# Kernel tuning notes

Hardware: AMD Instinct MI355X
Metric: run time of the kernel (lower is better)

Reference implementation:

```python
import jax, jax.numpy as jnp
import numpy as np

CONF_THRESH = 0.5   # foreground objectness threshold (module default)
NMS_THRESH = 0.4    # IoU suppression threshold (module default)
SCORE_THRESH = 0.3  # hard-coded max-class-score filter in forward

BS, NUM_BOXES, NUM_ATTRS = 2, 6300, 85  # 80 classes


def setup_inputs() -> dict:
    key = jax.random.key(0)
    # uniform [0,1): boxes live in the unit square and overlap heavily,
    # objectness/class scores frequently exceed the thresholds.
    x = jax.random.uniform(key, (BS, NUM_BOXES, NUM_ATTRS), dtype=jnp.float32)
    return {"x": x}


def _nms_keep(corners, scores, cls_idx, valid):
    """Per-image, per-class greedy NMS.

    corners: [N,4] (x1,y1,x2,y2), scores: [N] objectness, cls_idx: [N] int,
    valid: [N] bool. Returns keep mask [N] bool. Faithful to the torch loop:
    sort by objectness desc, greedily keep the top box of each class and
    suppress same-class boxes with IoU >= nms_thresh (torch keeps iou < t).
    """
    n = scores.shape[0]
    order = jnp.argsort(-scores)      # descending by objectness (column 4)
    rank = jnp.argsort(order)         # rank[j] = position of box j in order

    x1, y1, x2, y2 = corners[:, 0], corners[:, 1], corners[:, 2], corners[:, 3]
    area = (x2 - x1) * (y2 - y1)
    iw = jnp.maximum(jnp.minimum(x2[:, None], x2[None, :]) -
                     jnp.maximum(x1[:, None], x1[None, :]), 0.0)
    ih = jnp.maximum(jnp.minimum(y2[:, None], y2[None, :]) -
                     jnp.maximum(y1[:, None], y1[None, :]), 0.0)
    inter = iw * ih                                   # [N,N]
    iou = inter / (area[:, None] + area[None, :] - inter + 1e-16)
    same_cls = cls_idx[:, None] == cls_idx[None, :]    # [N,N]

    def body(r, keep):
        i = order[r]
        # suppress strictly lower-ranked, still-alive, same-class overlaps
        sup = (iou[i] >= NMS_THRESH) & same_cls[i] & (rank > r)
        return jnp.where(keep[i], keep & ~sup, keep)

    return jax.lax.fori_loop(0, n, body, valid)


def reference(x):
    """x: [bs, N, 5+num_classes]. Returns detections [bs, N, 8]:
    [batch_idx, x1, y1, x2, y2, p_obj, max_cls_score, cls_idx],
    zeroed for suppressed / filtered boxes (fixed-shape analogue of the
    variable-length torch output)."""
    conf_mask = x[..., 4] > CONF_THRESH
    xm = x * conf_mask[..., None].astype(x.dtype)

    # center -> corner transform
    xy, wh = xm[..., :2], xm[..., 2:4]
    corners = jnp.concatenate([xy - wh * 0.5, xy + wh * 0.5], axis=-1)  # [bs,N,4]

    p_obj = xm[..., 4]
    cls_scores = xm[..., 5:]
    max_score = jnp.max(cls_scores, axis=-1)
    cls_idx = jnp.argmax(cls_scores, axis=-1)
    valid = conf_mask & (max_score > SCORE_THRESH)

    keep = jax.vmap(_nms_keep)(corners, p_obj, cls_idx, valid)  # [bs,N] bool

    bs, n = p_obj.shape
    batch_idx = jnp.broadcast_to(
        jnp.arange(bs, dtype=x.dtype)[:, None], (bs, n))
    det = jnp.concatenate([
        batch_idx[..., None], corners, p_obj[..., None],
        max_score[..., None], cls_idx.astype(x.dtype)[..., None]], axis=-1)
    return det * keep[..., None].astype(x.dtype)
```

## Files before the change

kernel.cpp:

```cpp
#include <hip/hip_runtime.h>

#define BSZ   2
#define NBOX  6300
#define NATTR 85
#define NCLS  80
#define CAP   256

typedef unsigned long long ull;

static __device__ __forceinline__ ull mask_for(int rem) {
  if (rem <= 0) return 0ull;
  if (rem >= 64) return ~0ull;
  return (1ull << rem) - 1ull;
}

__global__ __launch_bounds__(256) void prep_kernel(
    const float* __restrict__ x,
    int* __restrict__ vcls,
    float* __restrict__ out) {
  int gid  = blockIdx.x * blockDim.x + threadIdx.x;
  int box  = gid >> 6;
  int lane = threadIdx.x & 63;

  const float* p = x + (long)box * NATTR;
  float r0 = p[lane];
  float r1 = (lane < NATTR - 64) ? p[64 + lane] : -1.0f;

  float c0 = (lane >= 5) ? r0 : -1.0f;
  float v; int vi;
  if (r1 > c0) { v = r1; vi = 64 + lane; }
  else         { v = c0; vi = lane; }

  for (int off = 32; off > 0; off >>= 1) {
    float ov = __shfl_xor(v, off);
    int   oi = __shfl_xor(vi, off);
    if (ov > v || (ov == v && oi < vi)) { v = ov; vi = oi; }
  }

  float cx  = __shfl(r0, 0), cy = __shfl(r0, 1);
  float w   = __shfl(r0, 2), h  = __shfl(r0, 3);
  float obj = __shfl(r0, 4);
  bool valid = (obj > 0.5f) && (v > 0.3f);
  int  img   = box >= NBOX ? 1 : 0;
  int  cls   = vi - 5;

  if (lane == 0) {
    vcls[box] = valid ? cls : -1;
    float4 a, b;
    if (valid) {
      float hw = w * 0.5f, hh = h * 0.5f;
      a = make_float4((float)img, cx - hw, cy - hh, cx + hw);
      b = make_float4(cy + hh, obj, v, (float)cls);
    } else {
      a = make_float4(0.f, 0.f, 0.f, 0.f);
      b = a;
    }
    float4* o = (float4*)(out + (long)box * 8);
    o[0] = a; o[1] = b;
  }
}

__global__ __launch_bounds__(256) void nms_kernel(
    const int* __restrict__ vcls,
    float* out) {
  __shared__ int   wlist[4][CAP];
  __shared__ int   wcnt[4];
  __shared__ int   sbi[CAP];
  __shared__ float ssc[CAP];
  __shared__ float px1[CAP], py1[CAP], px2[CAP], py2[CAP];
  __shared__ int   pbi[CAP];

  int bc   = blockIdx.x;
  int img  = bc / NCLS;
  int cls  = bc - img * NCLS;
  int t    = threadIdx.x;
  int lane = t & 63;
  int w    = t >> 6;
  const int* v = vcls + img * NBOX;

  int base = w * 1600;
  int vals[25];
#pragma unroll
  for (int i = 0; i < 25; i++) {
    int idx = base + i * 64 + lane;
    vals[i] = (idx < NBOX) ? v[idx] : -1;
  }
  int cnt = 0;
#pragma unroll
  for (int i = 0; i < 25; i++) {
    bool match = (vals[i] == cls);
    ull  m = __ballot(match);
    if (match) {
      int pos = cnt + __popcll(m & ((1ull << lane) - 1ull));
      if (pos < CAP) wlist[w][pos] = base + i * 64 + lane;
    }
    cnt += __popcll(m);
  }
  if (lane == 0) wcnt[w] = cnt < CAP ? cnt : CAP;
  __syncthreads();

  int off = 0, total = 0;
  for (int j = 0; j < 4; j++) {
    int c = wcnt[j];
    if (j < w) off += c;
    total += c;
  }
  int k = total < CAP ? total : CAP;
  if (k == 0) return;

  for (int j = lane; j < wcnt[w]; j += 64) {
    int d = off + j;
    if (d < CAP) sbi[d] = wlist[w][j];
  }
  __syncthreads();

  if (k <= 64) {
    if (w == 0) {
      int j = lane;
      float x1 = 0.f, y1 = 0.f, x2 = 0.f, y2 = 0.f, sc = 0.f;
      int bi = 0;
      if (j < k) {
        bi = sbi[j];
        const float4* o = (const float4*)(out + ((long)img * NBOX + bi) * 8);
        float4 a = o[0], b = o[1];
        x1 = a.y; y1 = a.z; x2 = a.w; y2 = b.x; sc = b.y;
      }
      int rank = 0;
      for (int i = 0; i < k; i++) {
        float si  = __shfl(sc, i);
        int   bii = __shfl(bi, i);
        rank += (si > sc) || (si == sc && bii < bi);
      }
      if (j >= k) rank = j;

      int r4 = rank << 2;
      x1 = __int_as_float(__builtin_amdgcn_ds_permute(r4, __float_as_int(x1)));
      y1 = __int_as_float(__builtin_amdgcn_ds_permute(r4, __float_as_int(y1)));
      x2 = __int_as_float(__builtin_amdgcn_ds_permute(r4, __float_as_int(x2)));
      y2 = __int_as_float(__builtin_amdgcn_ds_permute(r4, __float_as_int(y2)));
      bi = __builtin_amdgcn_ds_permute(r4, bi);

      float ar = (x2 - x1) * (y2 - y1);

      ull keep = mask_for(k);
      for (int r = 0; r < k - 1; r++) {
        if (!((keep >> r) & 1ull)) continue;
        float X1 = __shfl(x1, r), Y1 = __shfl(y1, r);
        float X2 = __shfl(x2, r), Y2 = __shfl(y2, r);
        float AR = __shfl(ar, r);
        float iw = fminf(X2, x2) - fmaxf(X1, x1);
        float ih = fminf(Y2, y2) - fmaxf(Y1, y1);
        iw = fmaxf(iw, 0.0f); ih = fmaxf(ih, 0.0f);
        float inter = iw * ih;
        float iou = inter / (AR + ar - inter + 1e-16f);
        keep &= ~__ballot(iou >= 0.4f && lane > r);
      }

      if (lane < k && !((keep >> lane) & 1ull)) {
        float4 z = make_float4(0.f, 0.f, 0.f, 0.f);
        float4* o = (float4*)(out + ((long)img * NBOX + bi) * 8);
        o[0] = z; o[1] = z;
      }
    }
    return;
  }

  float bx1 = 0, by1 = 0, bx2 = 0, by2 = 0, bobj = 0;
  int   bidx = 0;
  if (t < k) {
    bidx = sbi[t];
    const float4* o = (const float4*)(out + ((long)img * NBOX + bidx) * 8);
    float4 a = o[0], b = o[1];
    bx1 = a.y; by1 = a.z; bx2 = a.w; by2 = b.x; bobj = b.y;
    ssc[t] = bobj;
  }
  __syncthreads();

  if (t < k) {
    int rank = 0;
    for (int j = 0; j < k; j++) {
      float sj = ssc[j];
      rank += (sj > bobj) || (sj == bobj && sbi[j] < bidx);
    }
    px1[rank] = bx1; py1[rank] = by1;
    px2[rank] = bx2; py2[rank] = by2;
    pbi[rank] = bidx;
  }
  __syncthreads();

  if (w == 0) {
    float mx1[4], my1[4], mx2[4], my2[4], mar[4];
    int   mbi[4];
#pragma unroll
    for (int s = 0; s < 4; s++) {
      int e = s * 64 + lane;
      if (e < k) {
        mx1[s] = px1[e]; my1[s] = py1[e];
        mx2[s] = px2[e]; my2[s] = py2[e];
        mbi[s] = pbi[e];
        mar[s] = (mx2[s] - mx1[s]) * (my2[s] - my1[s]);
      } else {
        mx1[s] = 0; my1[s] = 0; mx2[s] = 0; my2[s] = 0; mar[s] = 0; mbi[s] = 0;
      }
    }
    ull km0 = mask_for(k);
    ull km1 = mask_for(k - 64);
    ull km2 = mask_for(k - 128);
    ull km3 = mask_for(k - 192);

    for (int r = 0; r < k - 1; r++) {
      ull cur = (r < 64) ? km0 : (r < 128) ? km1 : (r < 192) ? km2 : km3;
      if (!((cur >> (r & 63)) & 1ull)) continue;
      float X1 = px1[r], Y1 = py1[r], X2 = px2[r], Y2 = py2[r];
      float ar = (X2 - X1) * (Y2 - Y1);
      {
        int e = lane;
        float iw = fminf(X2, mx2[0]) - fmaxf(X1, mx1[0]);
        float ih = fminf(Y2, my2[0]) - fmaxf(Y1, my1[0]);
        iw = fmaxf(iw, 0.0f); ih = fmaxf(ih, 0.0f);
        float inter = iw * ih;
        float iou = inter / (ar + mar[0] - inter + 1e-16f);
        km0 &= ~__ballot(iou >= 0.4f && e > r && e < k);
      }
      if (k > 64) {
        int e = 64 + lane;
        float iw = fminf(X2, mx2[1]) - fmaxf(X1, mx1[1]);
        float ih = fminf(Y2, my2[1]) - fmaxf(Y1, my1[1]);
        iw = fmaxf(iw, 0.0f); ih = fmaxf(ih, 0.0f);
        float inter = iw * ih;
        float iou = inter / (ar + mar[1] - inter + 1e-16f);
        km1 &= ~__ballot(iou >= 0.4f && e > r && e < k);
      }
      if (k > 128) {
        int e = 128 + lane;
        float iw = fminf(X2, mx2[2]) - fmaxf(X1, mx1[2]);
        float ih = fminf(Y2, my2[2]) - fmaxf(Y1, my1[2]);
        iw = fmaxf(iw, 0.0f); ih = fmaxf(ih, 0.0f);
        float inter = iw * ih;
        float iou = inter / (ar + mar[2] - inter + 1e-16f);
        km2 &= ~__ballot(iou >= 0.4f && e > r && e < k);
      }
      if (k > 192) {
        int e = 192 + lane;
        float iw = fminf(X2, mx2[3]) - fmaxf(X1, mx1[3]);
        float ih = fminf(Y2, my2[3]) - fmaxf(Y1, my1[3]);
        iw = fmaxf(iw, 0.0f); ih = fmaxf(ih, 0.0f);
        float inter = iw * ih;
        float iou = inter / (ar + mar[3] - inter + 1e-16f);
        km3 &= ~__ballot(iou >= 0.4f && e > r && e < k);
      }
    }

    float4 z = make_float4(0.f, 0.f, 0.f, 0.f);
#pragma unroll
    for (int s = 0; s < 4; s++) {
      ull kms = (s == 0) ? km0 : (s == 1) ? km1 : (s == 2) ? km2 : km3;
      int e = s * 64 + lane;
      if (e < k && !((kms >> lane) & 1ull)) {
        float4* o = (float4*)(out + ((long)img * NBOX + mbi[s]) * 8);
        o[0] = z; o[1] = z;
      }
    }
  }
}

extern "C" void kernel_launch(void* const* d_in, const int* in_sizes, int n_in,
                              void* d_out, int out_size, void* d_ws, size_t ws_size,
                              hipStream_t stream) {
  const float* x = (const float*)d_in[0];
  float* out = (float*)d_out;
  int* vcls = (int*)d_ws;

  prep_kernel<<<(BSZ * NBOX * 64) / 256, 256, 0, stream>>>(x, vcls, out);
  nms_kernel<<<BSZ * NCLS, 256, 0, stream>>>(vcls, out);
}
```

Before: 69.56 us.

## Fuse prep and NMS into one cooperative kernel with atomic per-class lists

Merges the decode/filter pass and the per-class NMS pass into a single cooperative kernel separated by a grid-wide sync. During decode, valid boxes are appended to per-(image,class) lists with atomics, so the NMS phase no longer rescans all 6300 class ids per block. This removes one kernel launch and the full scan, but adds a memset launch, a grid barrier and atomic contention. Atomic insertion makes list order nondeterministic; the rank computation uses box index tie-breaks, so results should stay the same.

```diff
diff --git a/kernel.cpp b/kernel.cpp
--- a/kernel.cpp
+++ b/kernel.cpp
@@ -1,10 +1,15 @@
 #include <hip/hip_runtime.h>
+#include <hip/hip_cooperative_groups.h>
+
+namespace cg = cooperative_groups;
 
 #define BSZ   2
 #define NBOX  6300
 #define NATTR 85
 #define NCLS  80
 #define CAP   256
+#define NBLK  512
+#define NWAVES (NBLK * 4)
 
 typedef unsigned long long ull;
 
@@ -14,104 +19,75 @@
   return (1ull << rem) - 1ull;
 }
 
-__global__ __launch_bounds__(256) void prep_kernel(
+__global__ __launch_bounds__(256, 2) void fused_kernel(
     const float* __restrict__ x,
-    int* __restrict__ vcls,
-    float* __restrict__ out) {
-  int gid  = blockIdx.x * blockDim.x + threadIdx.x;
-  int box  = gid >> 6;
+    float* __restrict__ out,
+    int* __restrict__ cnt,
+    int* __restrict__ list) {
   int lane = threadIdx.x & 63;
-
-  const float* p = x + (long)box * NATTR;
-  float r0 = p[lane];
-  float r1 = (lane < NATTR - 64) ? p[64 + lane] : -1.0f;
-
-  float c0 = (lane >= 5) ? r0 : -1.0f;
-  float v; int vi;
-  if (r1 > c0) { v = r1; vi = 64 + lane; }
-  else         { v = c0; vi = lane; }
-
-  for (int off = 32; off > 0; off >>= 1) {
-    float ov = __shfl_xor(v, off);
-    int   oi = __shfl_xor(vi, off);
-    if (ov > v || (ov == v && oi < vi)) { v = ov; vi = oi; }
-  }
-
-  float cx  = __shfl(r0, 0), cy = __shfl(r0, 1);
-  float w   = __shfl(r0, 2), h  = __shfl(r0, 3);
-  float obj = __shfl(r0, 4);
-  bool valid = (obj > 0.5f) && (v > 0.3f);
-  int  img   = box >= NBOX ? 1 : 0;
-  int  cls   = vi - 5;
-
-  if (lane == 0) {
-    vcls[box] = valid ? cls : -1;
-    float4 a, b;
-    if (valid) {
-      float hw = w * 0.5f, hh = h * 0.5f;
-      a = make_float4((float)img, cx - hw, cy - hh, cx + hw);
-      b = make_float4(cy + hh, obj, v, (float)cls);
-    } else {
-      a = make_float4(0.f, 0.f, 0.f, 0.f);
-      b = a;
-    }
-    float4* o = (float4*)(out + (long)box * 8);
-    o[0] = a; o[1] = b;
-  }
-}
-
-__global__ __launch_bounds__(256) void nms_kernel(
-    const int* __restrict__ vcls,
-    float* out) {
-  __shared__ int   wlist[4][CAP];
-  __shared__ int   wcnt[4];
+  int gw   = (blockIdx.x * 256 + (int)threadIdx.x) >> 6;
+
+  for (int box = gw; box < BSZ * NBOX; box += NWAVES) {
+    const float* p = x + (long)box * NATTR;
+    float r0 = p[lane];
+    float r1 = (lane < NATTR - 64) ? p[64 + lane] : -1.0f;
+
+    float c0 = (lane >= 5) ? r0 : -1.0f;
+    float v; int vi;
+    if (r1 > c0) { v = r1; vi = 64 + lane; }
+    else         { v = c0; vi = lane; }
+
+    for (int off = 32; off > 0; off >>= 1) {
+      float ov = __shfl_xor(v, off);
+      int   oi = __shfl_xor(vi, off);
+      if (ov > v || (ov == v && oi < vi)) { v = ov; vi = oi; }
+    }
+
+    float cx  = __shfl(r0, 0), cy = __shfl(r0, 1);
+    float w   = __shfl(r0, 2), h  = __shfl(r0, 3);
+    float obj = __shfl(r0, 4);
+    bool valid = (obj > 0.5f) && (v > 0.3f);
+    int  img   = box >= NBOX ? 1 : 0;
+    int  bi    = box - img * NBOX;
+    int  cls   = vi - 5;
+
+    if (lane == 0) {
+      float4 a, b;
+      if (valid) {
+        float hw = w * 0.5f, hh = h * 0.5f;
+        a = make_float4((float)img, cx - hw, cy - hh, cx + hw);
+        b = make_float4(cy + hh, obj, v, (float)cls);
+        int li = img * NCLS + cls;
+        int slot = atomicAdd(&cnt[li], 1);
+        if (slot < CAP) list[li * CAP + slot] = bi;
+      } else {
+        a = make_float4(0.f, 0.f, 0.f, 0.f);
+        b = a;
+      }
+      float4* o = (float4*)(out + (long)box * 8);
+      o[0] = a; o[1] = b;
+    }
+  }
+
+  cg::this_grid().sync();
+
+  int bc = blockIdx.x;
+  if (bc >= BSZ * NCLS) return;
+
   __shared__ int   sbi[CAP];
   __shared__ float ssc[CAP];
   __shared__ float px1[CAP], py1[CAP], px2[CAP], py2[CAP];
   __shared__ int   pbi[CAP];
 
-  int bc   = blockIdx.x;
-  int img  = bc / NCLS;
-  int cls  = bc - img * NCLS;
-  int t    = threadIdx.x;
-  int lane = t & 63;
-  int w    = t >> 6;
-  const int* v = vcls + img * NBOX;
-
-  int base = w * 1600;
-  int vals[25];
-#pragma unroll
-  for (int i = 0; i < 25; i++) {
-    int idx = base + i * 64 + lane;
-    vals[i] = (idx < NBOX) ? v[idx] : -1;
-  }
-  int cnt = 0;
-#pragma unroll
-  for (int i = 0; i < 25; i++) {
-    bool match = (vals[i] == cls);
-    ull  m = __ballot(match);
-    if (match) {
-      int pos = cnt + __popcll(m & ((1ull << lane) - 1ull));
-      if (pos < CAP) wlist[w][pos] = base + i * 64 + lane;
-    }
-    cnt += __popcll(m);
-  }
-  if (lane == 0) wcnt[w] = cnt < CAP ? cnt : CAP;
-  __syncthreads();
-
-  int off = 0, total = 0;
-  for (int j = 0; j < 4; j++) {
-    int c = wcnt[j];
-    if (j < w) off += c;
-    total += c;
-  }
+  int img = bc / NCLS;
+  int t   = threadIdx.x;
+  int w   = t >> 6;
+
+  int total = cnt[bc];
   int k = total < CAP ? total : CAP;
   if (k == 0) return;
 
-  for (int j = lane; j < wcnt[w]; j += 64) {
-    int d = off + j;
-    if (d < CAP) sbi[d] = wlist[w][j];
-  }
+  for (int j = t; j < k; j += 256) sbi[j] = list[bc * CAP + j];
   __syncthreads();
 
   if (k <= 64) {
@@ -269,8 +245,12 @@
                               hipStream_t stream) {
   const float* x = (const float*)d_in[0];
   float* out = (float*)d_out;
-  int* vcls = (int*)d_ws;
-
-  prep_kernel<<<(BSZ * NBOX * 64) / 256, 256, 0, stream>>>(x, vcls, out);
-  nms_kernel<<<BSZ * NCLS, 256, 0, stream>>>(vcls, out);
+  int* cnt  = (int*)d_ws;
+  int* list = (int*)d_ws + 256;
+
+  hipMemsetAsync(cnt, 0, BSZ * NCLS * sizeof(int), stream);
+
+  void* args[] = { (void*)&x, (void*)&out, (void*)&cnt, (void*)&list };
+  hipLaunchCooperativeKernel((void*)fused_kernel, dim3(NBLK), dim3(256),
+                             args, 0, stream);
 }
```

Result: slower. 138.3 us (+98.8%).

## Fuse prep and NMS into one persistent kernel with global flag barrier

Applied to the files above, without the earlier changes.

Merges the preprocessing and per-class NMS kernels into a single launch of 160 blocks of 512 threads. Each block first decodes a strided share of boxes, then all blocks meet at a grid-wide barrier built from per-block magic-valued flags in workspace. After the barrier each block runs NMS for one image and class, using 8 waves to scan the class list. This removes one kernel launch and its gap, but it relies on all 160 blocks being co-resident, and a per-wave list capacity of 128 could overflow on skewed data.

```diff
diff --git a/kernel.cpp b/kernel.cpp
--- a/kernel.cpp
+++ b/kernel.cpp
@@ -5,6 +5,12 @@
 #define NATTR 85
 #define NCLS  80
 #define CAP   256
+#define TPB   512
+#define NW    8
+#define NBLK  (BSZ * NCLS)
+#define GWAVES (NBLK * NW)
+#define CHUNK 790
+#define WCAP  128
 
 typedef unsigned long long ull;
 
@@ -14,93 +20,123 @@
   return (1ull << rem) - 1ull;
 }
 
-__global__ __launch_bounds__(256) void prep_kernel(
+static __device__ __forceinline__ int magic_of(int b) {
+  return (int)(0xA53C9E1Du ^ ((unsigned)b * 0x9E3779B9u));
+}
+
+__global__ __launch_bounds__(TPB, 2) void nms_one(
     const float* __restrict__ x,
-    int* __restrict__ vcls,
-    float* __restrict__ out) {
-  int gid  = blockIdx.x * blockDim.x + threadIdx.x;
-  int box  = gid >> 6;
-  int lane = threadIdx.x & 63;
-
-  const float* p = x + (long)box * NATTR;
-  float r0 = p[lane];
-  float r1 = (lane < NATTR - 64) ? p[64 + lane] : -1.0f;
-
-  float c0 = (lane >= 5) ? r0 : -1.0f;
-  float v; int vi;
-  if (r1 > c0) { v = r1; vi = 64 + lane; }
-  else         { v = c0; vi = lane; }
-
-  for (int off = 32; off > 0; off >>= 1) {
-    float ov = __shfl_xor(v, off);
-    int   oi = __shfl_xor(vi, off);
-    if (ov > v || (ov == v && oi < vi)) { v = ov; vi = oi; }
-  }
-
-  float cx  = __shfl(r0, 0), cy = __shfl(r0, 1);
-  float w   = __shfl(r0, 2), h  = __shfl(r0, 3);
-  float obj = __shfl(r0, 4);
-  bool valid = (obj > 0.5f) && (v > 0.3f);
-  int  img   = box >= NBOX ? 1 : 0;
-  int  cls   = vi - 5;
-
-  if (lane == 0) {
-    vcls[box] = valid ? cls : -1;
-    float4 a, b;
-    if (valid) {
-      float hw = w * 0.5f, hh = h * 0.5f;
-      a = make_float4((float)img, cx - hw, cy - hh, cx + hw);
-      b = make_float4(cy + hh, obj, v, (float)cls);
-    } else {
-      a = make_float4(0.f, 0.f, 0.f, 0.f);
-      b = a;
-    }
-    float4* o = (float4*)(out + (long)box * 8);
-    o[0] = a; o[1] = b;
-  }
-}
-
-__global__ __launch_bounds__(256) void nms_kernel(
-    const int* __restrict__ vcls,
-    float* out) {
-  __shared__ int   wlist[4][CAP];
-  __shared__ int   wcnt[4];
+    float* __restrict__ out,
+    int* __restrict__ ws) {
+  int* vcls  = ws;
+  int* flags = ws + 12800;
+
+  __shared__ int   wlist[NW][WCAP];
+  __shared__ int   wcnt[NW];
   __shared__ int   sbi[CAP];
   __shared__ float ssc[CAP];
   __shared__ float px1[CAP], py1[CAP], px2[CAP], py2[CAP];
   __shared__ int   pbi[CAP];
 
-  int bc   = blockIdx.x;
-  int img  = bc / NCLS;
-  int cls  = bc - img * NCLS;
   int t    = threadIdx.x;
   int lane = t & 63;
   int w    = t >> 6;
+  int bid  = blockIdx.x;
+
+  for (int box = bid * NW + w; box < BSZ * NBOX; box += GWAVES) {
+    const float* p = x + (long)box * NATTR;
+    float r0 = p[lane];
+    float r1 = (lane < NATTR - 64) ? p[64 + lane] : -1.0f;
+
+    float c0 = (lane >= 5) ? r0 : -1.0f;
+    float v; int vi;
+    if (r1 > c0) { v = r1; vi = 64 + lane; }
+    else         { v = c0; vi = lane; }
+
+    for (int off = 32; off > 0; off >>= 1) {
+      float ov = __shfl_xor(v, off);
+      int   oi = __shfl_xor(vi, off);
+      if (ov > v || (ov == v && oi < vi)) { v = ov; vi = oi; }
+    }
+
+    float cx  = __shfl(r0, 0), cy = __shfl(r0, 1);
+    float ww  = __shfl(r0, 2), hh = __shfl(r0, 3);
+    float obj = __shfl(r0, 4);
+    bool valid = (obj > 0.5f) && (v > 0.3f);
+    int  img   = box >= NBOX ? 1 : 0;
+    int  cls   = vi - 5;
+
+    if (lane == 0) {
+      vcls[box] = valid ? cls : -1;
+      float4 a, b;
+      if (valid) {
+        float hw = ww * 0.5f, hh2 = hh * 0.5f;
+        a = make_float4((float)img, cx - hw, cy - hh2, cx + hw);
+        b = make_float4(cy + hh2, obj, v, (float)cls);
+      } else {
+        a = make_float4(0.f, 0.f, 0.f, 0.f);
+        b = a;
+      }
+      float4* o = (float4*)(out + (long)box * 8);
+      o[0] = a; o[1] = b;
+    }
+  }
+
+  __syncthreads();
+  __threadfence();
+  if (t == 0)
+    __hip_atomic_store(&flags[bid], magic_of(bid),
+                       __ATOMIC_RELEASE, __HIP_MEMORY_SCOPE_AGENT);
+  if (w == 0) {
+    int m0 = magic_of(lane);
+    int m1 = magic_of(64 + lane);
+    int m2 = (lane < 32) ? magic_of(128 + lane) : 0;
+    for (;;) {
+      int f0 = __hip_atomic_load(&flags[lane],
+                                 __ATOMIC_RELAXED, __HIP_MEMORY_SCOPE_AGENT);
+      int f1 = __hip_atomic_load(&flags[64 + lane],
+                                 __ATOMIC_RELAXED, __HIP_MEMORY_SCOPE_AGENT);
+      int f2 = (lane < 32)
+                 ? __hip_atomic_load(&flags[128 + lane],
+                                     __ATOMIC_RELAXED, __HIP_MEMORY_SCOPE_AGENT)
+                 : 0;
+      bool c = (f0 == m0) && (f1 == m1) && (lane >= 32 || f2 == m2);
+      if (__all(c)) break;
+      __builtin_amdgcn_s_sleep(8);
+    }
+    __threadfence();
+  }
+  __syncthreads();
+
+  int img = bid / NCLS;
+  int cls = bid - img * NCLS;
   const int* v = vcls + img * NBOX;
 
-  int base = w * 1600;
-  int vals[25];
+  int base = w * CHUNK;
+  int vals[13];
 #pragma unroll
-  for (int i = 0; i < 25; i++) {
-    int idx = base + i * 64 + lane;
-    vals[i] = (idx < NBOX) ? v[idx] : -1;
+  for (int i = 0; i < 13; i++) {
+    int local = i * 64 + lane;
+    int idx   = base + local;
+    vals[i] = (local < CHUNK && idx < NBOX) ? v[idx] : -1;
   }
   int cnt = 0;
+  ull lt = (1ull << lane) - 1ull;
 #pragma unroll
-  for (int i = 0; i < 25; i++) {
+  for (int i = 0; i < 13; i++) {
     bool match = (vals[i] == cls);
     ull  m = __ballot(match);
     if (match) {
-      int pos = cnt + __popcll(m & ((1ull << lane) - 1ull));
-      if (pos < CAP) wlist[w][pos] = base + i * 64 + lane;
+      int pos = cnt + __popcll(m & lt);
+      if (pos < WCAP) wlist[w][pos] = base + i * 64 + lane;
     }
     cnt += __popcll(m);
   }
-  if (lane == 0) wcnt[w] = cnt < CAP ? cnt : CAP;
+  if (lane == 0) wcnt[w] = cnt < WCAP ? cnt : WCAP;
   __syncthreads();
 
   int off = 0, total = 0;
-  for (int j = 0; j < 4; j++) {
+  for (int j = 0; j < NW; j++) {
     int c = wcnt[j];
     if (j < w) off += c;
     total += c;
@@ -269,8 +305,6 @@
                               hipStream_t stream) {
   const float* x = (const float*)d_in[0];
   float* out = (float*)d_out;
-  int* vcls = (int*)d_ws;
-
-  prep_kernel<<<(BSZ * NBOX * 64) / 256, 256, 0, stream>>>(x, vcls, out);
-  nms_kernel<<<BSZ * NCLS, 256, 0, stream>>>(vcls, out);
+  int* ws = (int*)d_ws;
+  nms_one<<<NBLK, TPB, 0, stream>>>(x, out, ws);
 }
```

After: 98.15 us. 1.41x slower.
